# Kernel tuning notes

Hardware: AMD Instinct MI355X
Metric: run time of the kernel (lower is better)

The kernel has to match this reference:

```python
import jax, jax.numpy as jnp
import numpy as np
from jax.scipy.special import ndtr, ndtri, logsumexp

M_FREQ = 50
N_LAYERS = 5
MIXTURE = 5
MU = 4.0 * np.pi * 1e-7
LOG_2PI = float(np.log(2.0 * np.pi))
BATCH = 131072
SAMPL = 1


def setup_inputs() -> dict:
    key = jax.random.key(0)
    k1, k2, k3, k4 = jax.random.split(key, 4)
    x = jax.random.uniform(k1, (BATCH, N_LAYERS + 2 * M_FREQ), jnp.float32)
    s = jax.random.normal(k2, (BATCH, MIXTURE, 2 * N_LAYERS + 1), jnp.float32)
    u_cat = jax.random.uniform(k3, (SAMPL, BATCH), jnp.float32)
    u_trunc = jax.random.uniform(k4, (SAMPL, BATCH, N_LAYERS), jnp.float32)
    return {"x": x, "s": s, "u_cat": u_cat, "u_trunc": u_trunc}


def _elbo(x, s, u_cat, u_trunc):
    n = N_LAYERS
    B = x.shape[0]
    freqs = jnp.asarray(10.0 ** np.linspace(-2, 3, M_FREQ), jnp.float32)
    # --- mixture-density head ---
    sq = jnp.square(s[:, :, 2 * n])
    pro = sq / jnp.sum(sq, axis=1, keepdims=True)              # [B, M] (fun_part_uni)
    sig = jax.nn.softplus(s[:, :, n:2 * n])                    # [B, M, n]
    loc = 4.0 * jax.nn.sigmoid(s[:, :, :n])                    # [B, M, n]
    # --- sample q = Mixture(TruncatedNormal(loc, sig, 0.1, 3.9)) via inverse CDF ---
    cum = jnp.cumsum(pro, axis=1)                              # [B, M]
    comp = jnp.clip(jnp.sum(u_cat[:, :, None] > cum[None], axis=-1), 0, MIXTURE - 1)  # [S,B] int
    b_idx = jnp.arange(B)[None, :]
    loc_s = loc[b_idx, comp]                                   # [S, B, n]
    sig_s = sig[b_idx, comp]
    a = (0.1 - loc_s) / sig_s
    b = (3.9 - loc_s) / sig_s
    Fa, Fb = ndtr(a), ndtr(b)
    z = ndtri(Fa + u_trunc * (Fb - Fa))
    samples_q = jnp.clip(loc_s + sig_s * z, 0.1, 3.9)          # [S, B, n]
    # --- FP: recursive MT impedance forward model, vectorized over frequencies ---
    thick = x[:, :n]                                            # [B, n]
    res = 10.0 ** samples_q                                     # [S, B, n]
    w = (2.0 * np.pi) * freqs[:, None, None]                    # [m, 1, 1]
    ZR = jnp.sqrt(w * MU * res[:, :, n - 1] / 2.0)              # [m, S, B]
    ZC = ZR
    for j in range(n - 2, -1, -1):
        rj = res[:, :, j]                                       # [S, B]
        th = thick[:, j]                                        # [B]
        dj = jnp.sqrt(w * MU * (1.0 / rj) / 2.0)                # [m, S, B]
        wj = dj * rj                                            # wjR == wjC in source
        t = 2.0 * th * dj
        e = jnp.exp(-t)
        ejR = e * jnp.cos(t)   # cos(-t) == cos(t)
        ejC = -e * jnp.sin(t)
        den = jnp.square(wj + ZR) + jnp.square(wj + ZC)
        rjR = (2.0 * jnp.square(wj) - jnp.square(ZR) - jnp.square(ZC)) / den
        rjC = (2.0 * wj * ZR - 2.0 * wj * ZC) / den
        reR = rjR * ejR - rjC * ejC
        reC = rjR * ejC + rjC * ejR
        den2 = jnp.square(1.0 + reR) + jnp.square(reC)
        auxR = (1.0 - jnp.square(reR) - jnp.square(reC)) / den2
        auxC = -(2.0 * reC) / den2
        ZR, ZC = wj * auxR - wj * auxC, wj * auxC + wj * auxR
    absZ2 = jnp.square(ZR) + jnp.square(ZC)                     # [m, S, B]
    aRes = jnp.log10(absZ2 / (MU * w))
    phas = jnp.arctan2(ZC, ZR)
    S = samples_q.shape[0]
    formation = jnp.transpose(jnp.concatenate([aRes, phas], 0), (2, 1, 0)).reshape(S, B, 2 * M_FREQ)
    # --- ELBO terms ---
    obs = x[:, n:]                                              # [B, 2m]
    scale = jnp.abs(0.03 * formation)
    v = formation - obs[None]
    ll = -0.5 * jnp.square(v / scale) - jnp.log(scale) - 0.5 * LOG_2PI
    term_lik = -jnp.mean(ll)
    # q_ : same mixture with bounds (0, 4), log-prob at samples_q
    a_ = (0.0 - loc) / sig
    b_ = (4.0 - loc) / sig
    zc = (samples_q[:, :, None, :] - loc[None]) / sig[None]     # [S, B, M, n]
    comp_lp = jnp.sum(
        -0.5 * jnp.square(zc) - 0.5 * LOG_2PI - jnp.log(sig)[None]
        - jnp.log(ndtr(b_) - ndtr(a_))[None], axis=-1)          # [S, B, M]
    lq = logsumexp(jnp.log(pro)[None] + comp_lp, axis=-1)
    term_q = jnp.mean(lq)
    term_p = -jnp.log(jnp.float32(4.0))  # Uniform(0,4).log_prob, constant
    return term_lik + term_q - term_p


def reference(x, s, u_cat, u_trunc):
    return _elbo(x, s, u_cat, u_trunc)
```

## Files before the change

kernel.cpp:

```cpp
#include <hip/hip_runtime.h>
#include <math.h>

#define NL 5
#define KM 5
#define MF 50
#define BATCH_ 131072
#define XROW (NL + 2*MF)
#define SROW (KM*(2*NL+1))
#define LOG2PI_F 1.8378770664093453f

#define BPB 64
#define NB_FUSED (BATCH_/BPB)

typedef float v2f __attribute__((ext_vector_type(2)));

__device__ __forceinline__ float rcpf_(float x)  { return __builtin_amdgcn_rcpf(x); }
__device__ __forceinline__ float sqrtf_(float x) { return __builtin_amdgcn_sqrtf(x); }
__device__ __forceinline__ float exp_(float x)   { return __expf(x); }
__device__ __forceinline__ float log_(float x)   { return __logf(x); }

__device__ __forceinline__ v2f ndtr2_f(v2f x) {
    v2f z = {fabsf(x.x), fabsf(x.y)};
    z = z * 0.70710678f;
    v2f td = 0.3275911f * z + 1.0f;
    v2f t  = {rcpf_(td.x), rcpf_(td.y)};
    v2f poly = t*(0.254829592f + t*(-0.284496736f + t*(1.421413741f +
               t*(-1.453152027f + t*1.061405429f))));
    v2f zz = z * z;
    v2f e  = {exp_(-zz.x), exp_(-zz.y)};
    v2f h  = 0.5f * poly * e;
    v2f r;
    r.x = x.x >= 0.0f ? 1.0f - h.x : h.x;
    r.y = x.y >= 0.0f ? 1.0f - h.y : h.y;
    return r;
}

__device__ __forceinline__ float ndtri_f(float p) {
    float x = fmaf(2.0f, p, -1.0f);
    float w = -log_((1.0f - x) * (1.0f + x));
    float wc = w - 2.5f;
    float pc =            2.81022636e-08f;
    pc = fmaf(pc, wc,     3.43273939e-07f);
    pc = fmaf(pc, wc,    -3.5233877e-06f);
    pc = fmaf(pc, wc,    -4.39150654e-06f);
    pc = fmaf(pc, wc,     0.00021858087f);
    pc = fmaf(pc, wc,    -0.00125372503f);
    pc = fmaf(pc, wc,    -0.00417768164f);
    pc = fmaf(pc, wc,     0.246640727f);
    pc = fmaf(pc, wc,     1.50140941f);
    float wt = sqrtf_(w) - 3.0f;
    float pt =           -0.000200214257f;
    pt = fmaf(pt, wt,     0.000100950558f);
    pt = fmaf(pt, wt,     0.00134934322f);
    pt = fmaf(pt, wt,    -0.00367342844f);
    pt = fmaf(pt, wt,     0.00573950773f);
    pt = fmaf(pt, wt,    -0.0076224613f);
    pt = fmaf(pt, wt,     0.00943887047f);
    pt = fmaf(pt, wt,     1.00167406f);
    pt = fmaf(pt, wt,     2.83297682f);
    float r = (w < 5.0f) ? pc : pt;
    return 1.41421356f * r * x;
}

__device__ __forceinline__ float atan2_f(float y, float x) {
    float ax = fabsf(x), ay = fabsf(y);
    float mx = fmaxf(ax, ay), mn = fminf(ax, ay);
    float a = mn * rcpf_(mx);
    float s = a * a;
    float r =            -0.01172120f;
    r = fmaf(r, s,        0.05265332f);
    r = fmaf(r, s,       -0.11643287f);
    r = fmaf(r, s,        0.19354346f);
    r = fmaf(r, s,       -0.33262347f);
    r = fmaf(r, s,        0.99997726f);
    r = r * a;
    r = (ay > ax)   ? (1.5707964f - r) : r;
    r = (x < 0.0f)  ? (3.1415927f - r) : r;
    return (y < 0.0f) ? -r : r;
}

__device__ __forceinline__ float fwd_eval2(v2f c5, v2f sw, v2f oA, v2f oP,
                                           const float pr[9])
{
    v2f z0 = sw * pr[0];
    v2f nR = z0, nC = z0;
    v2f dR = {1.0f, 1.0f}, dC = {0.0f, 0.0f};
    #pragma unroll
    for (int j = NL-2; j >= 0; --j) {
        v2f wj = sw * pr[5+j];
        v2f t  = sw * pr[1+j];
        v2f t2 = t * t, t3 = t2 * t;
        v2f ejR = (1.0f - t) + t3 * (0.33333334f - 0.16666667f * t);
        v2f ejC = t2 - 0.33333334f * t3 - t;
        v2f pRz = wj * (dR - dC);
        v2f pCz = wj * (dR + dC);
        v2f uR = pRz + nR, uC = pCz + nC;
        v2f vR = pRz - nR, vC = pCz - nC;
        v2f wR = ejR*vR - ejC*vC;
        v2f wC = ejR*vC + ejC*vR;
        v2f aR = uR - wR, aC = uC - wC;
        nR = wj * (aR - aC);
        nC = wj * (aR + aC);
        dR = uR + wR;
        dC = uC + wC;
    }
    v2f n2 = nR*nR + nC*nC;
    v2f d2 = dR*dR + dC*dC;
    v2f id2 = {rcpf_(d2.x), rcpf_(d2.y)};
    v2f absZ2 = n2 * id2;
    v2f mR = nR*dR + nC*dC;
    v2f mC = nC*dR - nR*dC;
    v2f aRes = {fmaf(0.43429448f, log_(absZ2.x), c5.x),
                fmaf(0.43429448f, log_(absZ2.y), c5.y)};
    v2f ph   = {atan2_f(mC.x, mR.x), atan2_f(mC.y, mR.y)};
    v2f prod = aRes * ph;
    v2f ap   = {fabsf(prod.x), fabsf(prod.y)};
    v2f invp = {rcpf_(ap.x), rcpf_(ap.y)};
    v2f aph  = {fabsf(ph.x),   fabsf(ph.y)};
    v2f aar  = {fabsf(aRes.x), fabsf(aRes.y)};
    v2f vA = (aRes - oA) * (33.333332f * aph * invp);
    v2f vP = (ph   - oP) * (33.333332f * aar * invp);
    v2f res = (v2f){5.1752387f - log_(ap.x), 5.1752387f - log_(ap.y)}
              - 0.5f*vA*vA - 0.5f*vP*vP;
    return res.x + res.y;
}

__device__ __forceinline__ float fwd_eval2x2(
    v2f c5a, v2f swa, v2f oAa, v2f oPa,
    v2f c5b, v2f swb, v2f oAb, v2f oPb,
    const float pr[9])
{
    v2f z0a = swa * pr[0];
    v2f z0b = swb * pr[0];
    v2f nRa = z0a, nCa = z0a, dRa = {1.0f,1.0f}, dCa = {0.0f,0.0f};
    v2f nRb = z0b, nCb = z0b, dRb = {1.0f,1.0f}, dCb = {0.0f,0.0f};
    #pragma unroll
    for (int j = NL-2; j >= 0; --j) {
        float p5 = pr[5+j], p1 = pr[1+j];
        v2f wja = swa * p5;            v2f wjb = swb * p5;
        v2f ta  = swa * p1;            v2f tb  = swb * p1;
        v2f t2a = ta * ta;             v2f t2b = tb * tb;
        v2f t3a = t2a * ta;            v2f t3b = t2b * tb;
        v2f ejRa = (1.0f - ta) + t3a * (0.33333334f - 0.16666667f * ta);
        v2f ejRb = (1.0f - tb) + t3b * (0.33333334f - 0.16666667f * tb);
        v2f ejCa = t2a - 0.33333334f * t3a - ta;
        v2f ejCb = t2b - 0.33333334f * t3b - tb;
        v2f pRa = wja * (dRa - dCa);   v2f pRb = wjb * (dRb - dCb);
        v2f pCa = wja * (dRa + dCa);   v2f pCb = wjb * (dRb + dCb);
        v2f uRa = pRa + nRa;           v2f uRb = pRb + nRb;
        v2f uCa = pCa + nCa;           v2f uCb = pCb + nCb;
        v2f vRa = pRa - nRa;           v2f vRb = pRb - nRb;
        v2f vCa = pCa - nCa;           v2f vCb = pCb - nCb;
        v2f wRa = ejRa*vRa - ejCa*vCa; v2f wRb = ejRb*vRb - ejCb*vCb;
        v2f wCa = ejRa*vCa + ejCa*vRa; v2f wCb = ejRb*vCb + ejCb*vRb;
        v2f aRa = uRa - wRa;           v2f aRb = uRb - wRb;
        v2f aCa = uCa - wCa;           v2f aCb = uCb - wCb;
        nRa = wja * (aRa - aCa);       nRb = wjb * (aRb - aCb);
        nCa = wja * (aRa + aCa);       nCb = wjb * (aRb + aCb);
        dRa = uRa + wRa;               dRb = uRb + wRb;
        dCa = uCa + wCa;               dCb = uCb + wCb;
    }
    v2f n2a = nRa*nRa + nCa*nCa;       v2f n2b = nRb*nRb + nCb*nCb;
    v2f d2a = dRa*dRa + dCa*dCa;       v2f d2b = dRb*dRb + dCb*dCb;
    v2f id2a = {rcpf_(d2a.x), rcpf_(d2a.y)};
    v2f id2b = {rcpf_(d2b.x), rcpf_(d2b.y)};
    v2f absZ2a = n2a * id2a;           v2f absZ2b = n2b * id2b;
    v2f mRa = nRa*dRa + nCa*dCa;       v2f mRb = nRb*dRb + nCb*dCb;
    v2f mCa = nCa*dRa - nRa*dCa;       v2f mCb = nCb*dRb - nRb*dCb;
    v2f aResa = {fmaf(0.43429448f, log_(absZ2a.x), c5a.x),
                 fmaf(0.43429448f, log_(absZ2a.y), c5a.y)};
    v2f aResb = {fmaf(0.43429448f, log_(absZ2b.x), c5b.x),
                 fmaf(0.43429448f, log_(absZ2b.y), c5b.y)};
    v2f pha = {atan2_f(mCa.x, mRa.x), atan2_f(mCa.y, mRa.y)};
    v2f phb = {atan2_f(mCb.x, mRb.x), atan2_f(mCb.y, mRb.y)};
    v2f proda = aResa * pha;           v2f prodb = aResb * phb;
    v2f apa = {fabsf(proda.x), fabsf(proda.y)};
    v2f apb = {fabsf(prodb.x), fabsf(prodb.y)};
    v2f invpa = {rcpf_(apa.x), rcpf_(apa.y)};
    v2f invpb = {rcpf_(apb.x), rcpf_(apb.y)};
    v2f apha = {fabsf(pha.x),   fabsf(pha.y)};
    v2f aphb = {fabsf(phb.x),   fabsf(phb.y)};
    v2f aara = {fabsf(aResa.x), fabsf(aResa.y)};
    v2f aarb = {fabsf(aResb.x), fabsf(aResb.y)};
    v2f vAa = (aResa - oAa) * (33.333332f * apha * invpa);
    v2f vAb = (aResb - oAb) * (33.333332f * aphb * invpb);
    v2f vPa = (pha   - oPa) * (33.333332f * aara * invpa);
    v2f vPb = (phb   - oPb) * (33.333332f * aarb * invpb);
    v2f resa = (v2f){5.1752387f - log_(apa.x), 5.1752387f - log_(apa.y)}
               - 0.5f*vAa*vAa - 0.5f*vPa*vPa;
    v2f resb = (v2f){5.1752387f - log_(apb.x), 5.1752387f - log_(apb.y)}
               - 0.5f*vAb*vAb - 0.5f*vPb*vPb;
    return (resa.x + resa.y) + (resb.x + resb.y);
}

__global__ void __launch_bounds__(256, 4) k_bnn(
    const float* __restrict__ x, const float* __restrict__ s,
    const float* __restrict__ u_cat, const float* __restrict__ u_trunc,
    float* __restrict__ out)
{
    __shared__ float lds_pr[BPB][12];
    __shared__ float red0[4], red1[4];

    unsigned tid = threadIdx.x;
    unsigned bl = tid >> 2;
    unsigned i  = tid & 3;
    unsigned b  = blockIdx.x * BPB + bl;
    const float* srow = s + (size_t)b * SROW;
    float lqv = 0.0f;

    float pro[KM];
    float sqsum = 0.0f;
    #pragma unroll
    for (int k = 0; k < KM; ++k) {
        float v = srow[k*11 + 10];
        pro[k] = v * v;
        sqsum += pro[k];
    }
    float isq = rcpf_(sqsum);
    #pragma unroll
    for (int k = 0; k < KM; ++k) pro[k] *= isq;
    float u = u_cat[b];
    float cum = 0.0f; int cnt = 0;
    #pragma unroll
    for (int k = 0; k < KM; ++k) { cum += pro[k]; if (u > cum) ++cnt; }
    int comp = cnt < KM-1 ? cnt : KM-1;

    float cacc[KM];
    #pragma unroll
    for (int k = 0; k < KM; ++k) cacc[k] = 0.0f;

    #pragma unroll
    for (int r = 0; r < 2; ++r) {
        unsigned layer = i + 4u*r;
        bool active = (layer < NL);
        unsigned ll_ = active ? layer : i;
        float lc[KM], sg[KM];
        #pragma unroll
        for (int k = 0; k < KM; ++k) {
            lc[k] = 4.0f * rcpf_(1.0f + exp_(-srow[k*11 + ll_]));
            float sv = srow[k*11 + 5 + ll_];
            sg[k] = fmaxf(sv, 0.0f) + log_(1.0f + exp_(-fabsf(sv)));
        }
        float ls = lc[0], ss = sg[0];
        #pragma unroll
        for (int k = 1; k < KM; ++k) {
            bool sel = (k == comp);
            ls = sel ? lc[k] : ls;
            ss = sel ? sg[k] : ss;
        }
        float invss = rcpf_(ss);
        float a  = (0.1f - ls) * invss;
        float bb = (3.9f - ls) * invss;
        v2f Fab = ndtr2_f((v2f){a, bb});
        float p  = Fab.x + u_trunc[(size_t)b*NL + ll_] * (Fab.y - Fab.x);
        p = fminf(fmaxf(p, 0.0f), 1.0f);
        float z = ndtri_f(p);
        if (p <= 0.0f) z = -INFINITY;
        if (p >= 1.0f) z =  INFINITY;
        float smp = fminf(fmaxf(fmaf(ss, z, ls), 0.1f), 3.9f);

        #pragma unroll
        for (int k = 0; k < KM; ++k) {
            float invs = rcpf_(sg[k]);
            float zc = (smp - lc[k]) * invs;
            float a_ = (-lc[k]) * invs;
            float b_ = (4.0f - lc[k]) * invs;
            v2f Fz = ndtr2_f((v2f){b_, a_});
            float Z  = Fz.x - Fz.y;
            float v  = fmaf(-0.5f, zc*zc, -0.5f*LOG2PI_F) - log_(sg[k] * Z);
            cacc[k] += active ? v : 0.0f;
        }
        const float SQM = 7.9267442e-04f;
        const float HLN10 = 1.1512925f;
        float em  = exp_(-HLN10 * smp);
        float emi = SQM * rcpf_(em);
        if (r == 0) {
            float th = x[(size_t)b*XROW + i];
            lds_pr[bl][1+i] = 2.0f * th * SQM * em;
            lds_pr[bl][5+i] = emi;
        } else if (active) {
            lds_pr[bl][0] = emi;
        }
    }
    #pragma unroll
    for (int k = 0; k < KM; ++k) {
        cacc[k] += __shfl_xor(cacc[k], 1, 4);
        cacc[k] += __shfl_xor(cacc[k], 2, 4);
    }
    {
        float mx = -INFINITY;
        float av[KM];
        #pragma unroll
        for (int k = 0; k < KM; ++k) { av[k] = log_(pro[k]) + cacc[k]; mx = fmaxf(mx, av[k]); }
        float se = 0.0f;
        #pragma unroll
        for (int k = 0; k < KM; ++k) se += exp_(av[k] - mx);
        if (i == 0) lqv = mx + log_(se);
    }
    __syncthreads();

    float pr[9];
    #pragma unroll
    for (int q = 0; q < 9; ++q) pr[q] = lds_pr[bl][q];
    const float* oAr = x + (size_t)b * XROW + NL;
    const float* oPr = oAr + MF;

    float ex0 = fmaf((float)i, 0.10204082f, -2.0f);
    v2f c5 = {5.1026102f - ex0, 5.1026102f - ex0 - 2.5510204f};
    v2f sw = {2.5066283f * exp_(1.1512925f * ex0),
              2.5066283f * exp_(1.1512925f * (ex0 + 2.5510204f))};
    const float SWP[6] = {1.0f, 1.5998587f, 2.5595479f,
                          4.0949150f, 6.5512855f, 10.4811311f};
    const float C5P[6] = {0.0f, 0.40816327f, 0.81632653f,
                          1.2244898f, 1.6326531f, 2.0408163f};
    float ll = 0.0f;
    #pragma unroll
    for (int q = 0; q < 3; ++q) {
        int m  = (int)i + 4*q;
        int m2 = m + 12;
        v2f oAa = {oAr[m],  oAr[m+25]};
        v2f oPa = {oPr[m],  oPr[m+25]};
        v2f oAb = {oAr[m2], oAr[m2+25]};
        v2f oPb = {oPr[m2], oPr[m2+25]};
        ll += fwd_eval2x2(c5 - C5P[q],   sw * SWP[q],   oAa, oPa,
                          c5 - C5P[q+3], sw * SWP[q+3], oAb, oPb, pr);
    }
    if (tid < 64) {
        unsigned bt = blockIdx.x * BPB + tid;
        float prt[9];
        #pragma unroll
        for (int q = 0; q < 9; ++q) prt[q] = lds_pr[tid][q];
        const float* xa = x + (size_t)bt * XROW + NL;
        float e24 = fmaf(24.0f, 0.10204082f, -2.0f);
        float e49 = fmaf(49.0f, 0.10204082f, -2.0f);
        v2f c5t = {5.1026102f - e24, 5.1026102f - e49};
        v2f swt = {2.5066283f * exp_(1.1512925f * e24),
                   2.5066283f * exp_(1.1512925f * e49)};
        v2f oAt = {xa[24], xa[49]};
        v2f oPt = {xa[MF + 24], xa[MF + 49]};
        ll += fwd_eval2(c5t, swt, oAt, oPt, prt);
    }

    #pragma unroll
    for (int off = 32; off > 0; off >>= 1) {
        ll  += __shfl_down(ll,  off, 64);
        lqv += __shfl_down(lqv, off, 64);
    }
    if ((tid & 63) == 0) {
        red0[tid >> 6] = ll;
        red1[tid >> 6] = lqv;
    }
    __syncthreads();
    if (tid == 0) {
        float llb = red0[0] + red0[1] + red0[2] + red0[3];
        float lqb = red1[0] + red1[1] + red1[2] + red1[3];
        float val = fmaf(llb, -7.62939453125e-8f, lqb * 7.62939453125e-6f);
        if (blockIdx.x == 0) val += 1.3862944f;
        atomicAdd(out, val);
    }
}

extern "C" void kernel_launch(void* const* d_in, const int* in_sizes, int n_in,
                              void* d_out, int out_size, void* d_ws, size_t ws_size,
                              hipStream_t stream)
{
    (void)in_sizes; (void)n_in; (void)out_size; (void)d_ws; (void)ws_size;
    const float* x       = (const float*)d_in[0];
    const float* s       = (const float*)d_in[1];
    const float* u_cat   = (const float*)d_in[2];
    const float* u_trunc = (const float*)d_in[3];
    float* out = (float*)d_out;

    k_bnn<<<NB_FUSED, 256, 0, stream>>>(x, s, u_cat, u_trunc, out);
}
```

Measured before the change: 132.3 us.

## Redistribute per-layer sampling work as flat cells across block threads

The per-(row, layer) sampling and mixture log-prob work is flattened into 320 cells per block. All 256 threads handle one cell, and only the first wave handles the remaining 64. Before, four threads per row each ran two padded passes, and most lanes in the second pass were idle. Per-component partial sums now go through LDS and are reduced per row after a barrier, and the tail frequency evaluation moves to the second wave to balance load. This costs extra LDS traffic, recomputes the mixture weights per cell, and adds a uniform-index gather of the s rows.

```diff
diff --git a/kernel.cpp b/kernel.cpp
--- a/kernel.cpp
+++ b/kernel.cpp
@@ -11,6 +11,7 @@
 
 #define BPB 64
 #define NB_FUSED (BATCH_/BPB)
+#define NCELL (BPB*NL)
 
 typedef float v2f __attribute__((ext_vector_type(2)));
 
@@ -193,11 +194,89 @@
     return (resa.x + resa.y) + (resb.x + resb.y);
 }
 
+__device__ __forceinline__ void process_cell(
+    unsigned c, unsigned block_b0,
+    const float* __restrict__ x, const float* __restrict__ s,
+    const float* __restrict__ u_cat, const float* __restrict__ u_trunc,
+    float lds_cc[BPB][NL][KM], float lds_pr[BPB][12])
+{
+    unsigned cb = c / NL;
+    unsigned cl = c - cb * NL;
+    unsigned b  = block_b0 + cb;
+    const float* srow = s + (size_t)b * SROW;
+
+    float pro[KM];
+    float sqsum = 0.0f;
+    #pragma unroll
+    for (int k = 0; k < KM; ++k) {
+        float v = srow[k*11 + 10];
+        pro[k] = v * v;
+        sqsum += pro[k];
+    }
+    float isq = rcpf_(sqsum);
+    #pragma unroll
+    for (int k = 0; k < KM; ++k) pro[k] *= isq;
+    float u = u_cat[b];
+    float cum = 0.0f; int cnt = 0;
+    #pragma unroll
+    for (int k = 0; k < KM; ++k) { cum += pro[k]; if (u > cum) ++cnt; }
+    int comp = cnt < KM-1 ? cnt : KM-1;
+
+    float lc[KM], sg[KM];
+    #pragma unroll
+    for (int k = 0; k < KM; ++k) {
+        lc[k] = 4.0f * rcpf_(1.0f + exp_(-srow[k*11 + cl]));
+        float sv = srow[k*11 + 5 + cl];
+        sg[k] = fmaxf(sv, 0.0f) + log_(1.0f + exp_(-fabsf(sv)));
+    }
+    float ls = lc[0], ss = sg[0];
+    #pragma unroll
+    for (int k = 1; k < KM; ++k) {
+        bool sel = (k == comp);
+        ls = sel ? lc[k] : ls;
+        ss = sel ? sg[k] : ss;
+    }
+    float invss = rcpf_(ss);
+    float a  = (0.1f - ls) * invss;
+    float bb = (3.9f - ls) * invss;
+    v2f Fab = ndtr2_f((v2f){a, bb});
+    float p  = Fab.x + u_trunc[(size_t)b*NL + cl] * (Fab.y - Fab.x);
+    p = fminf(fmaxf(p, 0.0f), 1.0f);
+    float z = ndtri_f(p);
+    if (p <= 0.0f) z = -INFINITY;
+    if (p >= 1.0f) z =  INFINITY;
+    float smp = fminf(fmaxf(fmaf(ss, z, ls), 0.1f), 3.9f);
+
+    #pragma unroll
+    for (int k = 0; k < KM; ++k) {
+        float invs = rcpf_(sg[k]);
+        float zc = (smp - lc[k]) * invs;
+        float a_ = (-lc[k]) * invs;
+        float b_ = (4.0f - lc[k]) * invs;
+        v2f Fz = ndtr2_f((v2f){b_, a_});
+        float Z  = Fz.x - Fz.y;
+        float v  = fmaf(-0.5f, zc*zc, -0.5f*LOG2PI_F) - log_(sg[k] * Z);
+        lds_cc[cb][cl][k] = v;
+    }
+    const float SQM = 7.9267442e-04f;
+    const float HLN10 = 1.1512925f;
+    float em  = exp_(-HLN10 * smp);
+    float emi = SQM * rcpf_(em);
+    if (cl == 4) {
+        lds_pr[cb][0] = emi;
+    } else {
+        float th = x[(size_t)b*XROW + cl];
+        lds_pr[cb][1+cl] = 2.0f * th * SQM * em;
+        lds_pr[cb][5+cl] = emi;
+    }
+}
+
 __global__ void __launch_bounds__(256, 4) k_bnn(
     const float* __restrict__ x, const float* __restrict__ s,
     const float* __restrict__ u_cat, const float* __restrict__ u_trunc,
     float* __restrict__ out)
 {
+    __shared__ float lds_cc[BPB][NL][KM];
     __shared__ float lds_pr[BPB][12];
     __shared__ float red0[4], red1[4];
 
@@ -205,99 +284,45 @@
     unsigned bl = tid >> 2;
     unsigned i  = tid & 3;
     unsigned b  = blockIdx.x * BPB + bl;
+    unsigned b0 = blockIdx.x * BPB;
     const float* srow = s + (size_t)b * SROW;
+
+    process_cell(tid, b0, x, s, u_cat, u_trunc, lds_cc, lds_pr);
+    if (tid < NCELL - 256) {
+        process_cell(256 + tid, b0, x, s, u_cat, u_trunc, lds_cc, lds_pr);
+    }
+    __syncthreads();
+
     float lqv = 0.0f;
-
-    float pro[KM];
-    float sqsum = 0.0f;
-    #pragma unroll
-    for (int k = 0; k < KM; ++k) {
-        float v = srow[k*11 + 10];
-        pro[k] = v * v;
-        sqsum += pro[k];
-    }
-    float isq = rcpf_(sqsum);
-    #pragma unroll
-    for (int k = 0; k < KM; ++k) pro[k] *= isq;
-    float u = u_cat[b];
-    float cum = 0.0f; int cnt = 0;
-    #pragma unroll
-    for (int k = 0; k < KM; ++k) { cum += pro[k]; if (u > cum) ++cnt; }
-    int comp = cnt < KM-1 ? cnt : KM-1;
-
-    float cacc[KM];
-    #pragma unroll
-    for (int k = 0; k < KM; ++k) cacc[k] = 0.0f;
-
-    #pragma unroll
-    for (int r = 0; r < 2; ++r) {
-        unsigned layer = i + 4u*r;
-        bool active = (layer < NL);
-        unsigned ll_ = active ? layer : i;
-        float lc[KM], sg[KM];
+    {
+        float cs[KM];
+        #pragma unroll
+        for (int k = 0; k < KM; ++k) cs[k] = 0.0f;
+        #pragma unroll
+        for (int l = 0; l < NL; ++l)
+            #pragma unroll
+            for (int k = 0; k < KM; ++k)
+                cs[k] += lds_cc[bl][l][k];
+        float prosq[KM]; float sqsum = 0.0f;
         #pragma unroll
         for (int k = 0; k < KM; ++k) {
-            lc[k] = 4.0f * rcpf_(1.0f + exp_(-srow[k*11 + ll_]));
-            float sv = srow[k*11 + 5 + ll_];
-            sg[k] = fmaxf(sv, 0.0f) + log_(1.0f + exp_(-fabsf(sv)));
+            float v = srow[k*11 + 10];
+            prosq[k] = v * v;
+            sqsum += prosq[k];
         }
-        float ls = lc[0], ss = sg[0];
-        #pragma unroll
-        for (int k = 1; k < KM; ++k) {
-            bool sel = (k == comp);
-            ls = sel ? lc[k] : ls;
-            ss = sel ? sg[k] : ss;
-        }
-        float invss = rcpf_(ss);
-        float a  = (0.1f - ls) * invss;
-        float bb = (3.9f - ls) * invss;
-        v2f Fab = ndtr2_f((v2f){a, bb});
-        float p  = Fab.x + u_trunc[(size_t)b*NL + ll_] * (Fab.y - Fab.x);
-        p = fminf(fmaxf(p, 0.0f), 1.0f);
-        float z = ndtri_f(p);
-        if (p <= 0.0f) z = -INFINITY;
-        if (p >= 1.0f) z =  INFINITY;
-        float smp = fminf(fmaxf(fmaf(ss, z, ls), 0.1f), 3.9f);
-
-        #pragma unroll
-        for (int k = 0; k < KM; ++k) {
-            float invs = rcpf_(sg[k]);
-            float zc = (smp - lc[k]) * invs;
-            float a_ = (-lc[k]) * invs;
-            float b_ = (4.0f - lc[k]) * invs;
-            v2f Fz = ndtr2_f((v2f){b_, a_});
-            float Z  = Fz.x - Fz.y;
-            float v  = fmaf(-0.5f, zc*zc, -0.5f*LOG2PI_F) - log_(sg[k] * Z);
-            cacc[k] += active ? v : 0.0f;
-        }
-        const float SQM = 7.9267442e-04f;
-        const float HLN10 = 1.1512925f;
-        float em  = exp_(-HLN10 * smp);
-        float emi = SQM * rcpf_(em);
-        if (r == 0) {
-            float th = x[(size_t)b*XROW + i];
-            lds_pr[bl][1+i] = 2.0f * th * SQM * em;
-            lds_pr[bl][5+i] = emi;
-        } else if (active) {
-            lds_pr[bl][0] = emi;
-        }
-    }
-    #pragma unroll
-    for (int k = 0; k < KM; ++k) {
-        cacc[k] += __shfl_xor(cacc[k], 1, 4);
-        cacc[k] += __shfl_xor(cacc[k], 2, 4);
-    }
-    {
+        float lsum = log_(sqsum);
         float mx = -INFINITY;
         float av[KM];
         #pragma unroll
-        for (int k = 0; k < KM; ++k) { av[k] = log_(pro[k]) + cacc[k]; mx = fmaxf(mx, av[k]); }
+        for (int k = 0; k < KM; ++k) {
+            av[k] = log_(prosq[k]) - lsum + cs[k];
+            mx = fmaxf(mx, av[k]);
+        }
         float se = 0.0f;
         #pragma unroll
         for (int k = 0; k < KM; ++k) se += exp_(av[k] - mx);
         if (i == 0) lqv = mx + log_(se);
     }
-    __syncthreads();
 
     float pr[9];
     #pragma unroll
@@ -325,11 +350,11 @@
         ll += fwd_eval2x2(c5 - C5P[q],   sw * SWP[q],   oAa, oPa,
                           c5 - C5P[q+3], sw * SWP[q+3], oAb, oPb, pr);
     }
-    if (tid < 64) {
-        unsigned bt = blockIdx.x * BPB + tid;
+    if (tid >= 64 && tid < 128) {
+        unsigned bt = b0 + (tid & 63);
         float prt[9];
         #pragma unroll
-        for (int q = 0; q < 9; ++q) prt[q] = lds_pr[tid][q];
+        for (int q = 0; q < 9; ++q) prt[q] = lds_pr[tid & 63][q];
         const float* xa = x + (size_t)bt * XROW + NL;
         float e24 = fmaf(24.0f, 0.10204082f, -2.0f);
         float e49 = fmaf(49.0f, 0.10204082f, -2.0f);
```

Result: no change. 132.0 us, median of 2 (-0.3%).
